# Optimization experiments

Hardware: AMD Instinct MI355X
Metric: run time of the kernel (lower is better)

The kernel has to match this reference:

```python
import jax, jax.numpy as jnp
import numpy as np

EMBED_DIM = 1024
NUM_HEADS = 16
HEAD_DIM = EMBED_DIM // NUM_HEADS


def setup_inputs() -> dict:
    key = jax.random.key(0)
    ks = jax.random.split(key, 5)
    T, B, E = 2048, 2, EMBED_DIM
    s = 1.0 / np.sqrt(E)
    return {
        "x": jax.random.normal(ks[0], (T, B, E), jnp.float32),
        "wq": jax.random.normal(ks[1], (E, E), jnp.float32) * s,
        "bq": jnp.zeros((E,), jnp.float32),
        "wk": jax.random.normal(ks[2], (E, E), jnp.float32) * s,
        "bk": jnp.zeros((E,), jnp.float32),
        "wv": jax.random.normal(ks[3], (E, E), jnp.float32) * s,
        "bv": jnp.zeros((E,), jnp.float32),
        "wo": jax.random.normal(ks[4], (E, E), jnp.float32) * s,
        "bo": jnp.zeros((E,), jnp.float32),
    }


def reference(x, wq, bq, wk, bk, wv, bv, wo, bo):
    # x: [T, B, E] (Time x Batch x Channel), self-attention: query = key = value = x
    T, B, E = x.shape
    H, D = NUM_HEADS, HEAD_DIM
    scaling = D ** -0.5
    # Linear projections (torch Linear: y = x @ W.T + b)
    q = (jnp.einsum('tbe,fe->tbf', x, wq) + bq) * scaling
    k = jnp.einsum('tbe,fe->tbf', x, wk) + bk
    v = jnp.einsum('tbe,fe->tbf', x, wv) + bv
    # reshape to [B*H, T, D] equivalent -> use [B, H, T, D]
    q = q.reshape(T, B, H, D).transpose(1, 2, 0, 3)  # [B,H,T,D]
    k = k.reshape(T, B, H, D).transpose(1, 2, 0, 3)
    v = v.reshape(T, B, H, D).transpose(1, 2, 0, 3)
    # scores: [B,H,T,S], fp32 softmax
    scores = jnp.einsum('bhtd,bhsd->bhts', q, k)
    probs = jax.nn.softmax(scores.astype(jnp.float32), axis=-1).astype(x.dtype)
    attn = jnp.einsum('bhts,bhsd->bhtd', probs, v)  # [B,H,T,D]
    attn = attn.transpose(2, 0, 1, 3).reshape(T, B, E)
    out = jnp.einsum('tbe,fe->tbf', attn, wo) + bo
    return out
```

## Files before the change

### kernel.cpp

```cpp
#include <hip/hip_runtime.h>
#include <cstddef>
#include <cstdint>

#define T_DIM 2048
#define E_DIM 1024
#define M_DIM 4096

typedef __attribute__((ext_vector_type(8))) short short8;
typedef __attribute__((ext_vector_type(8))) _Float16 half8;
typedef __attribute__((ext_vector_type(4))) _Float16 half4;
typedef __attribute__((ext_vector_type(4))) float f32x4;

__device__ __forceinline__ short f16_bits(float v) {
  return __builtin_bit_cast(short, (_Float16)v);
}
__device__ __forceinline__ unsigned int pk2(float a, float b) {
  return __builtin_bit_cast(unsigned int, __builtin_amdgcn_cvt_pkrtz(a, b));
}
__device__ __forceinline__ half8 h8(short8 s) { return __builtin_bit_cast(half8, s); }

__device__ __forceinline__ void gl_lds16(const short* g, const short* l) {
  __builtin_amdgcn_global_load_lds(
      (const __attribute__((address_space(1))) unsigned int*)g,
      (__attribute__((address_space(3))) unsigned int*)l, 16, 0, 0);
}

__global__ __launch_bounds__(256) void convert_all(
    const float* __restrict__ x, const float* __restrict__ wq,
    const float* __restrict__ wk, const float* __restrict__ wv,
    const float* __restrict__ wo,
    short* __restrict__ xh, short* __restrict__ wqh, short* __restrict__ wkh,
    short* __restrict__ wvh, short* __restrict__ woh)
{
  const int bid = blockIdx.x;
  const float* in; short* hi; int base;
  if (bid < 4096)      { in = x;  hi = xh;  base = 0;    }
  else if (bid < 5120) { in = wq; hi = wqh; base = 4096; }
  else if (bid < 6144) { in = wk; hi = wkh; base = 5120; }
  else if (bid < 7168) { in = wv; hi = wvh; base = 6144; }
  else                 { in = wo; hi = woh; base = 7168; }
  const int i = (bid - base) * 256 + threadIdx.x;
  float4 v = ((const float4*)in)[i];
  uint2 p;
  p.x = (unsigned short)f16_bits(v.x) | ((unsigned int)(unsigned short)f16_bits(v.y) << 16);
  p.y = (unsigned short)f16_bits(v.z) | ((unsigned int)(unsigned short)f16_bits(v.w) << 16);
  ((uint2*)hi)[i] = p;
}

__global__ __launch_bounds__(256) void gemm_qkv(
    const short* __restrict__ xh,
    const short* __restrict__ wqh, const short* __restrict__ wkh,
    const short* __restrict__ wvh,
    const float* __restrict__ bq, const float* __restrict__ bk,
    const float* __restrict__ bv,
    short* __restrict__ qo, short* __restrict__ ko, short* __restrict__ vto)
{
  __shared__ __align__(16) short smem[128 * 32 * 2];
  short* Ah = smem;
  short* Wh = smem + 128 * 32;
  const int tid = threadIdx.x;
  const int lane = tid & 63;
  const int w = tid >> 6;
  const int quad = lane >> 4;
  const int l15 = lane & 15;
  const int sel = blockIdx.x >> 3;
  const int n0 = (blockIdx.x & 7) * 128;
  const int m0 = blockIdx.y * 128;

  const short* wsel = sel == 0 ? wqh : sel == 1 ? wkh : wvh;
  const float* bias = sel == 0 ? bq : sel == 1 ? bk : bv;
  const float scale = sel == 0 ? 0.125f * 1.44269504088896f : 1.0f;

  const short* gsrc = (w < 2) ? xh : wsel;
  short* lbuf = (w < 2) ? Ah : Wh;
  const int rbase = (w < 2) ? m0 : n0;
  const int jb = (w & 1) * 4;
  const int lrow = lane >> 2;
  const int gphys = lane & 3;

  f32x4 zero = {0.f, 0.f, 0.f, 0.f};
  f32x4 acc[4][4];
#pragma unroll
  for (int i = 0; i < 4; ++i)
#pragma unroll
    for (int j = 0; j < 4; ++j) acc[i][j] = zero;

  const int wm = w & 1, wn = w >> 1;

  for (int k0 = 0; k0 < E_DIM; k0 += 32) {
    __syncthreads();
#pragma unroll
    for (int jj = 0; jj < 4; ++jj) {
      int j = jb + jj;
      int r = j * 16 + lrow;
      int gl = (gphys - (r >> 1)) & 3;
      gl_lds16(gsrc + (size_t)(rbase + r) * E_DIM + k0 + gl * 8, lbuf + j * 512);
    }
    __syncthreads();
    short8 ahf[4];
#pragma unroll
    for (int i = 0; i < 4; ++i) {
      int r = wm * 64 + i * 16 + l15;
      int idx = r * 32 + ((quad + (r >> 1)) & 3) * 8;
      ahf[i] = *(const short8*)&Ah[idx];
    }
#pragma unroll
    for (int j = 0; j < 4; ++j) {
      int r = wn * 64 + j * 16 + l15;
      int idx = r * 32 + ((quad + (r >> 1)) & 3) * 8;
      short8 bhf = *(const short8*)&Wh[idx];
#pragma unroll
      for (int i = 0; i < 4; ++i)
        acc[i][j] = __builtin_amdgcn_mfma_f32_16x16x32_f16(h8(ahf[i]), h8(bhf), acc[i][j], 0, 0, 0);
    }
  }

  if (sel < 2) {
#pragma unroll
    for (int j = 0; j < 4; ++j) {
      const int gc = n0 + wn * 64 + j * 16 + l15;
      const float bb = bias[gc];
      const int h = gc >> 6, d = gc & 63;
      short* dst = sel == 0 ? qo : ko;
#pragma unroll
      for (int i = 0; i < 4; ++i)
#pragma unroll
        for (int reg = 0; reg < 4; ++reg) {
          const int gm = m0 + wm * 64 + i * 16 + quad * 4 + reg;
          const float val = (acc[i][j][reg] + bb) * scale;
          const int t = gm >> 1, b = gm & 1;
          dst[((size_t)(b * 16 + h) * T_DIM + t) * 64 + d] = f16_bits(val);
        }
    }
  } else {
    short* Tb = smem;
    const int by = blockIdx.y;
#pragma unroll
    for (int R = 0; R < 2; ++R) {
      __syncthreads();
      if (wn == R) {
#pragma unroll
        for (int j = 0; j < 4; ++j) {
          const int nl = j * 16 + l15;
          const int gc = n0 + R * 64 + nl;
          const float bb = bias[gc];
#pragma unroll
          for (int i = 0; i < 4; ++i) {
            const int tp = wm * 32 + i * 8 + quad * 2;
            unsigned int lo = pk2(acc[i][j][0] + bb, acc[i][j][2] + bb);
            unsigned int hi = pk2(acc[i][j][1] + bb, acc[i][j][3] + bb);
            const int g0 = tp >> 3;
            const int sub = tp & 7;
            *(unsigned int*)&Tb[nl * 128 + ((g0 + nl) & 15) * 8 + sub] = lo;
            *(unsigned int*)&Tb[nl * 128 + ((g0 + 8 + nl) & 15) * 8 + sub] = hi;
          }
        }
      }
      __syncthreads();
#pragma unroll
      for (int ii = 0; ii < 4; ++ii) {
        const int n = w * 16 + ii * 4 + quad;
        const int g = (l15 - n) & 15;
        short8 vvec = *(const short8*)&Tb[n * 128 + l15 * 8];
        const int gc = n0 + R * 64 + n;
        const int h = gc >> 6, d = gc & 63;
        const int b = g >> 3;
        const int t = by * 64 + (g & 7) * 8;
        *(short8*)&vto[((size_t)(b * 16 + h) * 64 + d) * T_DIM + t] = vvec;
      }
    }
  }
}

__global__ __launch_bounds__(256) void gemm_out(
    const short* __restrict__ attn, const short* __restrict__ woh,
    const float* __restrict__ bo, float* __restrict__ out)
{
  __shared__ __align__(16) short Ah[128 * 32], Wh[128 * 32];
  const int tid = threadIdx.x;
  const int lane = tid & 63;
  const int w = tid >> 6;
  const int quad = lane >> 4;
  const int l15 = lane & 15;
  const int n0 = blockIdx.x * 128;
  const int m0 = blockIdx.y * 128;

  const short* gsrc = (w < 2) ? attn : woh;
  short* lbuf = (w < 2) ? Ah : Wh;
  const int rbase = (w < 2) ? m0 : n0;
  const int jb = (w & 1) * 4;
  const int lrow = lane >> 2;
  const int gphys = lane & 3;

  f32x4 zero = {0.f, 0.f, 0.f, 0.f};
  f32x4 acc[4][4];
#pragma unroll
  for (int i = 0; i < 4; ++i)
#pragma unroll
    for (int j = 0; j < 4; ++j) acc[i][j] = zero;

  const int wm = w & 1, wn = w >> 1;

  for (int k0 = 0; k0 < E_DIM; k0 += 32) {
    __syncthreads();
#pragma unroll
    for (int jj = 0; jj < 4; ++jj) {
      int j = jb + jj;
      int r = j * 16 + lrow;
      int gl = (gphys - (r >> 1)) & 3;
      gl_lds16(gsrc + (size_t)(rbase + r) * E_DIM + k0 + gl * 8, lbuf + j * 512);
    }
    __syncthreads();
    short8 ahf[4];
#pragma unroll
    for (int i = 0; i < 4; ++i) {
      int r = wm * 64 + i * 16 + l15;
      int idx = r * 32 + ((quad + (r >> 1)) & 3) * 8;
      ahf[i] = *(const short8*)&Ah[idx];
    }
#pragma unroll
    for (int j = 0; j < 4; ++j) {
      int r = wn * 64 + j * 16 + l15;
      int idx = r * 32 + ((quad + (r >> 1)) & 3) * 8;
      short8 bhf = *(const short8*)&Wh[idx];
#pragma unroll
      for (int i = 0; i < 4; ++i)
        acc[i][j] = __builtin_amdgcn_mfma_f32_16x16x32_f16(h8(ahf[i]), h8(bhf), acc[i][j], 0, 0, 0);
    }
  }

#pragma unroll
  for (int j = 0; j < 4; ++j) {
    const int gc = n0 + wn * 64 + j * 16 + l15;
    const float bb = bo[gc];
#pragma unroll
    for (int i = 0; i < 4; ++i)
#pragma unroll
      for (int reg = 0; reg < 4; ++reg) {
        const int gm = m0 + wm * 64 + i * 16 + quad * 4 + reg;
        out[(size_t)gm * E_DIM + gc] = acc[i][j][reg] + bb;
      }
  }
}

__global__ __launch_bounds__(256, 2) void attn_mfma(
    const short* __restrict__ q, const short* __restrict__ k,
    const short* __restrict__ vt, short* __restrict__ attn)
{
  __shared__ __align__(16) short SMEM[32768];
  __shared__ float l_red[4][128];
  short* Qs = SMEM;
  short* KV = SMEM + 8192;

  const int tid = threadIdx.x;
  const int lane = tid & 63;
  const int w = tid >> 6;
  const int quad = lane >> 4;
  const int l15 = lane & 15;
  const int bhid = blockIdx.y;
  const int b = bhid >> 4, h = bhid & 15;
  const int t0 = blockIdx.x * 128;

  const short* qb = q + (size_t)bhid * T_DIM * 64;
  const short* kb = k + (size_t)bhid * T_DIM * 64;
  const short* vb = vt + (size_t)bhid * 64 * T_DIM;

  const int lrow8 = lane >> 3;
  const int gph8 = lane & 7;

#pragma unroll
  for (int jj = 0; jj < 4; ++jj) {
    int j = w * 4 + jj;
    int r = j * 8 + lrow8;
    int gl = (gph8 - (r >> 1)) & 7;
    gl_lds16(qb + (size_t)(t0 + r) * 64 + gl * 8, Qs + j * 512);
  }

  const int kg = (gph8 - lrow8) & 7;
  const int vd = lane >> 1, vh = lane & 1;
#pragma unroll
  for (int c0 = 0; c0 < 2; ++c0) {
    short* slot = KV + c0 * 8192 + w * 2048;
    const int sg = c0 * 64 + w * 16;
    gl_lds16(kb + (size_t)(sg + lrow8) * 64 + kg * 8, slot);
    gl_lds16(kb + (size_t)(sg + lrow8 + 8) * 64 + kg * 8, slot + 512);
    gl_lds16(vb + (size_t)vd * T_DIM + sg + vh * 8, slot + 1024);
    gl_lds16(vb + (size_t)(vd + 32) * T_DIM + sg + vh * 8, slot + 1536);
  }
  __syncthreads();

  short8 qa[8][2];
#pragma unroll
  for (int qbk = 0; qbk < 8; ++qbk)
#pragma unroll
    for (int st = 0; st < 2; ++st) {
      int r = qbk * 16 + l15;
      int idx = r * 64 + (((st * 4 + quad) + (r >> 1)) & 7) * 8;
      qa[qbk][st] = *(const short8*)&Qs[idx];
    }

  f32x4 zero = {0.f, 0.f, 0.f, 0.f};
  f32x4 acc[4][8];
  float l_part[8];
#pragma unroll
  for (int d = 0; d < 4; ++d)
#pragma unroll
    for (int qb2 = 0; qb2 < 8; ++qb2) acc[d][qb2] = zero;
#pragma unroll
  for (int i = 0; i < 8; ++i) l_part[i] = 0.f;

  for (int c = 0; c < 32; ++c) {
    if (c >= 2) {
      if (c == 31) __builtin_amdgcn_s_waitcnt(0x0F70);
      else         __builtin_amdgcn_s_waitcnt(0x0F74);
    }
    const short* slot = KV + (c % 3) * 8192 + w * 2048;

    short8 kf[2];
#pragma unroll
    for (int st = 0; st < 2; ++st)
      kf[st] = *(const short8*)&slot[l15 * 64 + (((st * 4 + quad) + l15) & 7) * 8];
    uint2 vfu[4];
#pragma unroll
    for (int dblk = 0; dblk < 4; ++dblk)
      vfu[dblk] = *(const uint2*)&slot[1024 + (dblk * 16 + l15) * 16 + quad * 4];

    if (c < 30) {
      short* nslot = KV + ((c + 2) % 3) * 8192 + w * 2048;
      const int sg = (c + 2) * 64 + w * 16;
      gl_lds16(kb + (size_t)(sg + lrow8) * 64 + kg * 8, nslot);
      gl_lds16(kb + (size_t)(sg + lrow8 + 8) * 64 + kg * 8, nslot + 512);
      gl_lds16(vb + (size_t)vd * T_DIM + sg + vh * 8, nslot + 1024);
      gl_lds16(vb + (size_t)(vd + 32) * T_DIM + sg + vh * 8, nslot + 1536);
    }

    uint2 pb[8];
#pragma unroll
    for (int qbk = 0; qbk < 8; ++qbk) {
      f32x4 s = zero;
      s = __builtin_amdgcn_mfma_f32_16x16x32_f16(h8(kf[0]), h8(qa[qbk][0]), s, 0, 0, 0);
      s = __builtin_amdgcn_mfma_f32_16x16x32_f16(h8(kf[1]), h8(qa[qbk][1]), s, 0, 0, 0);
      float p0 = __builtin_amdgcn_exp2f(s[0]);
      float p1 = __builtin_amdgcn_exp2f(s[1]);
      float p2 = __builtin_amdgcn_exp2f(s[2]);
      float p3 = __builtin_amdgcn_exp2f(s[3]);
      l_part[qbk] += (p0 + p1) + (p2 + p3);
      pb[qbk].x = pk2(p0, p1);
      pb[qbk].y = pk2(p2, p3);
    }

#pragma unroll
    for (int dblk = 0; dblk < 4; ++dblk) {
      half4 va = __builtin_bit_cast(half4, vfu[dblk]);
#pragma unroll
      for (int qbk = 0; qbk < 8; ++qbk)
        acc[dblk][qbk] = __builtin_amdgcn_mfma_f32_16x16x16f16(
            va, __builtin_bit_cast(half4, pb[qbk]), acc[dblk][qbk], 0, 0, 0);
    }
  }

#pragma unroll
  for (int qbk = 0; qbk < 8; ++qbk) {
    float l = l_part[qbk];
    l += __shfl_xor(l, 16);
    l += __shfl_xor(l, 32);
    if (quad == 0) l_red[w][qbk * 16 + l15] = l;
  }

  f32x4* Osc = (f32x4*)SMEM;
  __syncthreads();
  if (w & 1) {
    f32x4* dst = Osc + (w >> 1) * 2048;
#pragma unroll
    for (int dblk = 0; dblk < 4; ++dblk)
#pragma unroll
      for (int qbk = 0; qbk < 8; ++qbk)
        dst[(dblk * 8 + qbk) * 64 + lane] = acc[dblk][qbk];
  }
  __syncthreads();
  if (!(w & 1)) {
    f32x4* src = Osc + (w >> 1) * 2048;
#pragma unroll
    for (int dblk = 0; dblk < 4; ++dblk)
#pragma unroll
      for (int qbk = 0; qbk < 8; ++qbk) {
        f32x4 t = src[(dblk * 8 + qbk) * 64 + lane];
        acc[dblk][qbk][0] += t[0]; acc[dblk][qbk][1] += t[1];
        acc[dblk][qbk][2] += t[2]; acc[dblk][qbk][3] += t[3];
      }
  }
  __syncthreads();
  if (w == 2) {
#pragma unroll
    for (int dblk = 0; dblk < 4; ++dblk)
#pragma unroll
      for (int qbk = 0; qbk < 8; ++qbk)
        Osc[(dblk * 8 + qbk) * 64 + lane] = acc[dblk][qbk];
  }
  __syncthreads();
  if (w == 0) {
#pragma unroll
    for (int qbk = 0; qbk < 8; ++qbk) {
      const int qq = qbk * 16 + l15;
      const float lsum = l_red[0][qq] + l_red[1][qq] + l_red[2][qq] + l_red[3][qq];
      const float inv = 1.f / lsum;
      const int t = t0 + qq;
      const size_t mrow = (size_t)(t * 2 + b) * E_DIM;
#pragma unroll
      for (int dblk = 0; dblk < 4; ++dblk) {
        f32x4 t4 = Osc[(dblk * 8 + qbk) * 64 + lane];
        float a0 = acc[dblk][qbk][0] + t4[0];
        float a1 = acc[dblk][qbk][1] + t4[1];
        float a2 = acc[dblk][qbk][2] + t4[2];
        float a3 = acc[dblk][qbk][3] + t4[3];
        uint2 ov;
        ov.x = pk2(a0 * inv, a1 * inv);
        ov.y = pk2(a2 * inv, a3 * inv);
        *(uint2*)&attn[mrow + h * 64 + dblk * 16 + quad * 4] = ov;
      }
    }
  }
}

extern "C" void kernel_launch(void* const* d_in, const int* in_sizes, int n_in,
                              void* d_out, int out_size, void* d_ws, size_t ws_size,
                              hipStream_t stream)
{
  const float* x  = (const float*)d_in[0];
  const float* wq = (const float*)d_in[1];
  const float* bq = (const float*)d_in[2];
  const float* wk = (const float*)d_in[3];
  const float* bk = (const float*)d_in[4];
  const float* wv = (const float*)d_in[5];
  const float* bv = (const float*)d_in[6];
  const float* wo = (const float*)d_in[7];
  const float* bo = (const float*)d_in[8];
  float* out = (float*)d_out;

  short* ws = (short*)d_ws;
  const size_t M4 = (size_t)M_DIM * E_DIM;
  const size_t M1 = (size_t)E_DIM * E_DIM;
  short* xh   = ws;
  short* wqh  = xh + M4;
  short* wkh  = wqh + M1;
  short* wvh  = wkh + M1;
  short* woh  = wvh + M1;
  short* qws  = woh + M1;
  short* kws  = qws + M4;
  short* vtws = kws + M4;
  short* aws  = vtws + M4;

  convert_all<<<8192, 256, 0, stream>>>(x, wq, wk, wv, wo, xh, wqh, wkh, wvh, woh);
  gemm_qkv<<<dim3(24, 32), 256, 0, stream>>>(xh, wqh, wkh, wvh, bq, bk, bv,
                                             qws, kws, vtws);
  attn_mfma<<<dim3(16, 32), 256, 0, stream>>>(qws, kws, vtws, aws);
  gemm_out<<<dim3(8, 32), 256, 0, stream>>>(aws, woh, bo, out);
}
```

Measured before the change: 202.8 us.

## Split-K output GEMM, shrink attention LDS ring for higher occupancy

The attention kernel's LDS footprint shrinks by aliasing the Q staging buffer into the K/V triple-buffer ring, adding a barrier after Q is read into registers. Launch bounds rise from 2 to 3 blocks per CU. The cross-wave accumulator reduction is rewritten as a three-round pairwise exchange, so two waves write output instead of one. The output projection is split along K into two partial GEMMs (512 blocks instead of 256), followed by a new kernel that sums the partials and adds the bias. This costs extra fp32 partial writes and a separate pass, in exchange for better CU fill; the partial buffers reuse workspace that held the converted inputs.

```diff
diff --git a/kernel.cpp b/kernel.cpp
--- a/kernel.cpp
+++ b/kernel.cpp
@@ -174,7 +174,7 @@
 
 __global__ __launch_bounds__(256) void gemm_out(
     const short* __restrict__ attn, const short* __restrict__ woh,
-    const float* __restrict__ bo, float* __restrict__ out)
+    float* __restrict__ p0, float* __restrict__ p1)
 {
   __shared__ __align__(16) short Ah[128 * 32], Wh[128 * 32];
   const int tid = threadIdx.x;
@@ -184,6 +184,8 @@
   const int l15 = lane & 15;
   const int n0 = blockIdx.x * 128;
   const int m0 = blockIdx.y * 128;
+  const int z = blockIdx.z;
+  float* part = z ? p1 : p0;
 
   const short* gsrc = (w < 2) ? attn : woh;
   short* lbuf = (w < 2) ? Ah : Wh;
@@ -201,7 +203,7 @@
 
   const int wm = w & 1, wn = w >> 1;
 
-  for (int k0 = 0; k0 < E_DIM; k0 += 32) {
+  for (int k0 = z * 512; k0 < z * 512 + 512; k0 += 32) {
     __syncthreads();
 #pragma unroll
     for (int jj = 0; jj < 4; ++jj) {
@@ -232,25 +234,37 @@
 #pragma unroll
   for (int j = 0; j < 4; ++j) {
     const int gc = n0 + wn * 64 + j * 16 + l15;
-    const float bb = bo[gc];
 #pragma unroll
     for (int i = 0; i < 4; ++i)
 #pragma unroll
       for (int reg = 0; reg < 4; ++reg) {
         const int gm = m0 + wm * 64 + i * 16 + quad * 4 + reg;
-        out[(size_t)gm * E_DIM + gc] = acc[i][j][reg] + bb;
+        part[(size_t)gm * E_DIM + gc] = acc[i][j][reg];
       }
   }
 }
 
-__global__ __launch_bounds__(256, 2) void attn_mfma(
+__global__ __launch_bounds__(256) void add_bias(
+    const float* __restrict__ p0, const float* __restrict__ p1,
+    const float* __restrict__ bo, float* __restrict__ out)
+{
+  const int i = blockIdx.x * 256 + threadIdx.x;
+  const int col = (i * 4) & (E_DIM - 1);
+  float4 a = ((const float4*)p0)[i];
+  float4 b = ((const float4*)p1)[i];
+  float4 c = *(const float4*)&bo[col];
+  float4 o;
+  o.x = a.x + b.x + c.x; o.y = a.y + b.y + c.y;
+  o.z = a.z + b.z + c.z; o.w = a.w + b.w + c.w;
+  ((float4*)out)[i] = o;
+}
+
+__global__ __launch_bounds__(256, 3) void attn_mfma(
     const short* __restrict__ q, const short* __restrict__ k,
     const short* __restrict__ vt, short* __restrict__ attn)
 {
-  __shared__ __align__(16) short SMEM[32768];
+  __shared__ __align__(16) short SMEM[24576];
   __shared__ float l_red[4][128];
-  short* Qs = SMEM;
-  short* KV = SMEM + 8192;
 
   const int tid = threadIdx.x;
   const int lane = tid & 63;
@@ -267,6 +281,8 @@
 
   const int lrow8 = lane >> 3;
   const int gph8 = lane & 7;
+  short* Qs = SMEM;
+  const int ring_off[3] = {8192, 16384, 0};
 
 #pragma unroll
   for (int jj = 0; jj < 4; ++jj) {
@@ -280,7 +296,7 @@
   const int vd = lane >> 1, vh = lane & 1;
 #pragma unroll
   for (int c0 = 0; c0 < 2; ++c0) {
-    short* slot = KV + c0 * 8192 + w * 2048;
+    short* slot = SMEM + ring_off[c0] + w * 2048;
     const int sg = c0 * 64 + w * 16;
     gl_lds16(kb + (size_t)(sg + lrow8) * 64 + kg * 8, slot);
     gl_lds16(kb + (size_t)(sg + lrow8 + 8) * 64 + kg * 8, slot + 512);
@@ -298,6 +314,7 @@
       int idx = r * 64 + (((st * 4 + quad) + (r >> 1)) & 7) * 8;
       qa[qbk][st] = *(const short8*)&Qs[idx];
     }
+  __syncthreads();
 
   f32x4 zero = {0.f, 0.f, 0.f, 0.f};
   f32x4 acc[4][8];
@@ -314,7 +331,7 @@
       if (c == 31) __builtin_amdgcn_s_waitcnt(0x0F70);
       else         __builtin_amdgcn_s_waitcnt(0x0F74);
     }
-    const short* slot = KV + (c % 3) * 8192 + w * 2048;
+    const short* slot = SMEM + ring_off[c % 3] + w * 2048;
 
     short8 kf[2];
 #pragma unroll
@@ -326,7 +343,7 @@
       vfu[dblk] = *(const uint2*)&slot[1024 + (dblk * 16 + l15) * 16 + quad * 4];
 
     if (c < 30) {
-      short* nslot = KV + ((c + 2) % 3) * 8192 + w * 2048;
+      short* nslot = SMEM + ring_off[(c + 2) % 3] + w * 2048;
       const int sg = (c + 2) * 64 + w * 16;
       gl_lds16(kb + (size_t)(sg + lrow8) * 64 + kg * 8, nslot);
       gl_lds16(kb + (size_t)(sg + lrow8 + 8) * 64 + kg * 8, nslot + 512);
@@ -366,39 +383,53 @@
     l += __shfl_xor(l, 32);
     if (quad == 0) l_red[w][qbk * 16 + l15] = l;
   }
-
-  f32x4* Osc = (f32x4*)SMEM;
   __syncthreads();
-  if (w & 1) {
-    f32x4* dst = Osc + (w >> 1) * 2048;
-#pragma unroll
-    for (int dblk = 0; dblk < 4; ++dblk)
-#pragma unroll
-      for (int qbk = 0; qbk < 8; ++qbk)
-        dst[(dblk * 8 + qbk) * 64 + lane] = acc[dblk][qbk];
-  }
-  __syncthreads();
-  if (!(w & 1)) {
-    f32x4* src = Osc + (w >> 1) * 2048;
-#pragma unroll
-    for (int dblk = 0; dblk < 4; ++dblk)
-#pragma unroll
-      for (int qbk = 0; qbk < 8; ++qbk) {
-        f32x4 t = src[(dblk * 8 + qbk) * 64 + lane];
-        acc[dblk][qbk][0] += t[0]; acc[dblk][qbk][1] += t[1];
-        acc[dblk][qbk][2] += t[2]; acc[dblk][qbk][3] += t[3];
-      }
-  }
-  __syncthreads();
-  if (w == 2) {
-#pragma unroll
-    for (int dblk = 0; dblk < 4; ++dblk)
-#pragma unroll
-      for (int qbk = 0; qbk < 8; ++qbk)
-        Osc[(dblk * 8 + qbk) * 64 + lane] = acc[dblk][qbk];
-  }
-  __syncthreads();
-  if (w == 0) {
+
+  f32x4* R0 = (f32x4*)SMEM;
+  f32x4* R1 = R0 + 1024;
+  const int w01[3] = {1, 2, 3};
+  const int w23[3] = {3, 0, 1};
+#pragma unroll
+  for (int rnd = 0; rnd < 3; ++rnd) {
+    if (w == w01[rnd]) {
+#pragma unroll
+      for (int d2 = 0; d2 < 2; ++d2)
+#pragma unroll
+        for (int qbk = 0; qbk < 8; ++qbk)
+          R0[(d2 * 8 + qbk) * 64 + lane] = acc[d2][qbk];
+    }
+    if (w == w23[rnd]) {
+#pragma unroll
+      for (int d2 = 0; d2 < 2; ++d2)
+#pragma unroll
+        for (int qbk = 0; qbk < 8; ++qbk)
+          R1[(d2 * 8 + qbk) * 64 + lane] = acc[2 + d2][qbk];
+    }
+    __syncthreads();
+    if (w == 0) {
+#pragma unroll
+      for (int d2 = 0; d2 < 2; ++d2)
+#pragma unroll
+        for (int qbk = 0; qbk < 8; ++qbk) {
+          f32x4 t = R0[(d2 * 8 + qbk) * 64 + lane];
+          acc[d2][qbk][0] += t[0]; acc[d2][qbk][1] += t[1];
+          acc[d2][qbk][2] += t[2]; acc[d2][qbk][3] += t[3];
+        }
+    }
+    if (w == 2) {
+#pragma unroll
+      for (int d2 = 0; d2 < 2; ++d2)
+#pragma unroll
+        for (int qbk = 0; qbk < 8; ++qbk) {
+          f32x4 t = R1[(d2 * 8 + qbk) * 64 + lane];
+          acc[2 + d2][qbk][0] += t[0]; acc[2 + d2][qbk][1] += t[1];
+          acc[2 + d2][qbk][2] += t[2]; acc[2 + d2][qbk][3] += t[3];
+        }
+    }
+    __syncthreads();
+  }
+
+  if (w == 0 || w == 2) {
 #pragma unroll
     for (int qbk = 0; qbk < 8; ++qbk) {
       const int qq = qbk * 16 + l15;
@@ -407,15 +438,11 @@
       const int t = t0 + qq;
       const size_t mrow = (size_t)(t * 2 + b) * E_DIM;
 #pragma unroll
-      for (int dblk = 0; dblk < 4; ++dblk) {
-        f32x4 t4 = Osc[(dblk * 8 + qbk) * 64 + lane];
-        float a0 = acc[dblk][qbk][0] + t4[0];
-        float a1 = acc[dblk][qbk][1] + t4[1];
-        float a2 = acc[dblk][qbk][2] + t4[2];
-        float a3 = acc[dblk][qbk][3] + t4[3];
+      for (int d2 = 0; d2 < 2; ++d2) {
+        const int dblk = w + d2;
         uint2 ov;
-        ov.x = pk2(a0 * inv, a1 * inv);
-        ov.y = pk2(a2 * inv, a3 * inv);
+        ov.x = pk2(acc[dblk][qbk][0] * inv, acc[dblk][qbk][1] * inv);
+        ov.y = pk2(acc[dblk][qbk][2] * inv, acc[dblk][qbk][3] * inv);
         *(uint2*)&attn[mrow + h * 64 + dblk * 16 + quad * 4] = ov;
       }
     }
@@ -440,19 +467,22 @@
   short* ws = (short*)d_ws;
   const size_t M4 = (size_t)M_DIM * E_DIM;
   const size_t M1 = (size_t)E_DIM * E_DIM;
-  short* xh   = ws;
+  short* aws  = ws;
+  short* woh  = aws + M4;
+  short* xh   = woh + M1;
   short* wqh  = xh + M4;
   short* wkh  = wqh + M1;
   short* wvh  = wkh + M1;
-  short* woh  = wvh + M1;
-  short* qws  = woh + M1;
+  short* qws  = wvh + M1;
   short* kws  = qws + M4;
   short* vtws = kws + M4;
-  short* aws  = vtws + M4;
+  float* part0 = (float*)xh;
+  float* part1 = part0 + M4;
 
   convert_all<<<8192, 256, 0, stream>>>(x, wq, wk, wv, wo, xh, wqh, wkh, wvh, woh);
   gemm_qkv<<<dim3(24, 32), 256, 0, stream>>>(xh, wqh, wkh, wvh, bq, bk, bv,
                                              qws, kws, vtws);
   attn_mfma<<<dim3(16, 32), 256, 0, stream>>>(qws, kws, vtws, aws);
-  gemm_out<<<dim3(8, 32), 256, 0, stream>>>(aws, woh, bo, out);
-}
+  gemm_out<<<dim3(8, 32, 2), 256, 0, stream>>>(aws, woh, part0, part1);
+  add_bias<<<4096, 256, 0, stream>>>(part0, part1, bo, out);
+}
```

Result: slower. 440.1 us (+117.0%).

## Double GEMM K-tile to 64 and split-K output projection with bias-add kernel

Applied to the files above, without the earlier changes.

Both the QKV and output GEMMs now stage 64-wide K tiles in LDS with an 8-way XOR-style swizzle, halving the number of barrier-separated load/compute iterations. The output projection, which had only 256 blocks, is split along K into two halves writing fp32 partials. The partials reuse the dead x/weight fp16 workspace, and a new elementwise kernel sums them and adds the bias. This raises parallelism on the small GEMM to fill more CUs. The cost is extra partial-sum traffic to memory and one more kernel launch.

```diff
diff --git a/kernel.cpp b/kernel.cpp
--- a/kernel.cpp
+++ b/kernel.cpp
@@ -55,9 +55,9 @@
     const float* __restrict__ bv,
     short* __restrict__ qo, short* __restrict__ ko, short* __restrict__ vto)
 {
-  __shared__ __align__(16) short smem[128 * 32 * 2];
+  __shared__ __align__(16) short smem[128 * 64 * 2];
   short* Ah = smem;
-  short* Wh = smem + 128 * 32;
+  short* Wh = smem + 8192;
   const int tid = threadIdx.x;
   const int lane = tid & 63;
   const int w = tid >> 6;
@@ -74,9 +74,9 @@
   const short* gsrc = (w < 2) ? xh : wsel;
   short* lbuf = (w < 2) ? Ah : Wh;
   const int rbase = (w < 2) ? m0 : n0;
-  const int jb = (w & 1) * 4;
-  const int lrow = lane >> 2;
-  const int gphys = lane & 3;
+  const int lrow8 = lane >> 3;
+  const int gph8 = lane & 7;
+  const int kg = (gph8 - lrow8) & 7;
 
   f32x4 zero = {0.f, 0.f, 0.f, 0.f};
   f32x4 acc[4][4];
@@ -87,31 +87,31 @@
 
   const int wm = w & 1, wn = w >> 1;
 
-  for (int k0 = 0; k0 < E_DIM; k0 += 32) {
+  for (int k0 = 0; k0 < E_DIM; k0 += 64) {
     __syncthreads();
 #pragma unroll
-    for (int jj = 0; jj < 4; ++jj) {
-      int j = jb + jj;
-      int r = j * 16 + lrow;
-      int gl = (gphys - (r >> 1)) & 3;
-      gl_lds16(gsrc + (size_t)(rbase + r) * E_DIM + k0 + gl * 8, lbuf + j * 512);
+    for (int jj = 0; jj < 8; ++jj) {
+      int j = (w & 1) * 8 + jj;
+      int r = j * 8 + lrow8;
+      gl_lds16(gsrc + (size_t)(rbase + r) * E_DIM + k0 + kg * 8, lbuf + j * 512);
     }
     __syncthreads();
-    short8 ahf[4];
-#pragma unroll
-    for (int i = 0; i < 4; ++i) {
-      int r = wm * 64 + i * 16 + l15;
-      int idx = r * 32 + ((quad + (r >> 1)) & 3) * 8;
-      ahf[i] = *(const short8*)&Ah[idx];
-    }
-#pragma unroll
-    for (int j = 0; j < 4; ++j) {
-      int r = wn * 64 + j * 16 + l15;
-      int idx = r * 32 + ((quad + (r >> 1)) & 3) * 8;
-      short8 bhf = *(const short8*)&Wh[idx];
-#pragma unroll
-      for (int i = 0; i < 4; ++i)
-        acc[i][j] = __builtin_amdgcn_mfma_f32_16x16x32_f16(h8(ahf[i]), h8(bhf), acc[i][j], 0, 0, 0);
+#pragma unroll
+    for (int ks = 0; ks < 2; ++ks) {
+      short8 ahf[4];
+#pragma unroll
+      for (int i = 0; i < 4; ++i) {
+        int r = wm * 64 + i * 16 + l15;
+        ahf[i] = *(const short8*)&Ah[r * 64 + ((ks * 4 + quad + r) & 7) * 8];
+      }
+#pragma unroll
+      for (int j = 0; j < 4; ++j) {
+        int r = wn * 64 + j * 16 + l15;
+        short8 bhf = *(const short8*)&Wh[r * 64 + ((ks * 4 + quad + r) & 7) * 8];
+#pragma unroll
+        for (int i = 0; i < 4; ++i)
+          acc[i][j] = __builtin_amdgcn_mfma_f32_16x16x32_f16(h8(ahf[i]), h8(bhf), acc[i][j], 0, 0, 0);
+      }
     }
   }
 
@@ -174,9 +174,11 @@
 
 __global__ __launch_bounds__(256) void gemm_out(
     const short* __restrict__ attn, const short* __restrict__ woh,
-    const float* __restrict__ bo, float* __restrict__ out)
-{
-  __shared__ __align__(16) short Ah[128 * 32], Wh[128 * 32];
+    float* __restrict__ p0, float* __restrict__ p1)
+{
+  __shared__ __align__(16) short smem[128 * 64 * 2];
+  short* Ah = smem;
+  short* Wh = smem + 8192;
   const int tid = threadIdx.x;
   const int lane = tid & 63;
   const int w = tid >> 6;
@@ -184,13 +186,15 @@
   const int l15 = lane & 15;
   const int n0 = blockIdx.x * 128;
   const int m0 = blockIdx.y * 128;
+  const int z = blockIdx.z;
+  float* part = z ? p1 : p0;
 
   const short* gsrc = (w < 2) ? attn : woh;
   short* lbuf = (w < 2) ? Ah : Wh;
   const int rbase = (w < 2) ? m0 : n0;
-  const int jb = (w & 1) * 4;
-  const int lrow = lane >> 2;
-  const int gphys = lane & 3;
+  const int lrow8 = lane >> 3;
+  const int gph8 = lane & 7;
+  const int kg = (gph8 - lrow8) & 7;
 
   f32x4 zero = {0.f, 0.f, 0.f, 0.f};
   f32x4 acc[4][4];
@@ -201,46 +205,60 @@
 
   const int wm = w & 1, wn = w >> 1;
 
-  for (int k0 = 0; k0 < E_DIM; k0 += 32) {
+  for (int k0 = z * 512; k0 < z * 512 + 512; k0 += 64) {
     __syncthreads();
 #pragma unroll
-    for (int jj = 0; jj < 4; ++jj) {
-      int j = jb + jj;
-      int r = j * 16 + lrow;
-      int gl = (gphys - (r >> 1)) & 3;
-      gl_lds16(gsrc + (size_t)(rbase + r) * E_DIM + k0 + gl * 8, lbuf + j * 512);
+    for (int jj = 0; jj < 8; ++jj) {
+      int j = (w & 1) * 8 + jj;
+      int r = j * 8 + lrow8;
+      gl_lds16(gsrc + (size_t)(rbase + r) * E_DIM + k0 + kg * 8, lbuf + j * 512);
     }
     __syncthreads();
-    short8 ahf[4];
-#pragma unroll
-    for (int i = 0; i < 4; ++i) {
-      int r = wm * 64 + i * 16 + l15;
-      int idx = r * 32 + ((quad + (r >> 1)) & 3) * 8;
-      ahf[i] = *(const short8*)&Ah[idx];
-    }
-#pragma unroll
-    for (int j = 0; j < 4; ++j) {
-      int r = wn * 64 + j * 16 + l15;
-      int idx = r * 32 + ((quad + (r >> 1)) & 3) * 8;
-      short8 bhf = *(const short8*)&Wh[idx];
-#pragma unroll
-      for (int i = 0; i < 4; ++i)
-        acc[i][j] = __builtin_amdgcn_mfma_f32_16x16x32_f16(h8(ahf[i]), h8(bhf), acc[i][j], 0, 0, 0);
+#pragma unroll
+    for (int ks = 0; ks < 2; ++ks) {
+      short8 ahf[4];
+#pragma unroll
+      for (int i = 0; i < 4; ++i) {
+        int r = wm * 64 + i * 16 + l15;
+        ahf[i] = *(const short8*)&Ah[r * 64 + ((ks * 4 + quad + r) & 7) * 8];
+      }
+#pragma unroll
+      for (int j = 0; j < 4; ++j) {
+        int r = wn * 64 + j * 16 + l15;
+        short8 bhf = *(const short8*)&Wh[r * 64 + ((ks * 4 + quad + r) & 7) * 8];
+#pragma unroll
+        for (int i = 0; i < 4; ++i)
+          acc[i][j] = __builtin_amdgcn_mfma_f32_16x16x32_f16(h8(ahf[i]), h8(bhf), acc[i][j], 0, 0, 0);
+      }
     }
   }
 
 #pragma unroll
   for (int j = 0; j < 4; ++j) {
     const int gc = n0 + wn * 64 + j * 16 + l15;
-    const float bb = bo[gc];
 #pragma unroll
     for (int i = 0; i < 4; ++i)
 #pragma unroll
       for (int reg = 0; reg < 4; ++reg) {
         const int gm = m0 + wm * 64 + i * 16 + quad * 4 + reg;
-        out[(size_t)gm * E_DIM + gc] = acc[i][j][reg] + bb;
-      }
-  }
+        part[(size_t)gm * E_DIM + gc] = acc[i][j][reg];
+      }
+  }
+}
+
+__global__ __launch_bounds__(256) void add_bias(
+    const float* __restrict__ p0, const float* __restrict__ p1,
+    const float* __restrict__ bo, float* __restrict__ out)
+{
+  const int i = blockIdx.x * 256 + threadIdx.x;
+  const int col = (i * 4) & (E_DIM - 1);
+  float4 a = ((const float4*)p0)[i];
+  float4 b = ((const float4*)p1)[i];
+  float4 c = *(const float4*)&bo[col];
+  float4 o;
+  o.x = a.x + b.x + c.x; o.y = a.y + b.y + c.y;
+  o.z = a.z + b.z + c.z; o.w = a.w + b.w + c.w;
+  ((float4*)out)[i] = o;
 }
 
 __global__ __launch_bounds__(256, 2) void attn_mfma(
@@ -440,19 +458,22 @@
   short* ws = (short*)d_ws;
   const size_t M4 = (size_t)M_DIM * E_DIM;
   const size_t M1 = (size_t)E_DIM * E_DIM;
-  short* xh   = ws;
+  short* aws  = ws;
+  short* woh  = aws + M4;
+  short* xh   = woh + M1;
   short* wqh  = xh + M4;
   short* wkh  = wqh + M1;
   short* wvh  = wkh + M1;
-  short* woh  = wvh + M1;
-  short* qws  = woh + M1;
+  short* qws  = wvh + M1;
   short* kws  = qws + M4;
   short* vtws = kws + M4;
-  short* aws  = vtws + M4;
+  float* part0 = (float*)xh;
+  float* part1 = part0 + M4;
 
   convert_all<<<8192, 256, 0, stream>>>(x, wq, wk, wv, wo, xh, wqh, wkh, wvh, woh);
   gemm_qkv<<<dim3(24, 32), 256, 0, stream>>>(xh, wqh, wkh, wvh, bq, bk, bv,
                                              qws, kws, vtws);
   attn_mfma<<<dim3(16, 32), 256, 0, stream>>>(qws, kws, vtws, aws);
-  gemm_out<<<dim3(8, 32), 256, 0, stream>>>(aws, woh, bo, out);
-}
+  gemm_out<<<dim3(8, 32, 2), 256, 0, stream>>>(aws, woh, part0, part1);
+  add_bias<<<4096, 256, 0, stream>>>(part0, part1, bo, out);
+}
```

New measurement: 204.0 us. About the same (+0.6%).
